# Optimization experiments

Hardware: AMD Instinct MI355X
Metric: run time of the kernel (lower is better)

The kernel has to match this reference:

```python
import jax, jax.numpy as jnp
import numpy as np

K = 1000   # grid rows (detections from model 1, truncated to 1000)
N = 1000   # grid cols (detections from model 2)
M = 900000 # number of non-empty (overlapping) pairs
F = 7      # per-pair feature dim
SENTINEL = -9999.0


def setup_inputs() -> dict:
    key = jax.random.key(0)
    ks = jax.random.split(key, 12)
    def w(k, o, i):
        return jax.random.normal(k, (o, i), dtype=jnp.float32) * 0.05
    def b(k, o):
        return jax.random.normal(k, (o,), dtype=jnp.float32) * 0.05
    return {
        "input_1": jax.random.normal(ks[0], (1, F, 1, M), dtype=jnp.float32),
        "T_out": jnp.zeros((1, K, N), dtype=jnp.float32),
        "T_indices": jax.random.randint(ks[1], (2, M), 0, K),
        "w1": w(ks[2], 18, F),  "b1": b(ks[3], 18),
        "w2": w(ks[4], 36, 18), "b2": b(ks[5], 36),
        "w3": w(ks[6], 36, 36), "b3": b(ks[7], 36),
        "w4": w(ks[8], 1, 36),  "b4": b(ks[9], 1),
    }


def reference(input_1, T_out, T_indices, w1, b1, w2, b2, w3, b3, w4, b4):
    # 1x1 conv stack == channel matmuls on the flattened [F, M] features.
    x = input_1[0, :, 0, :]                       # [F, M]
    h = jax.nn.relu(w1 @ x + b1[:, None])         # [18, M]
    h = jax.nn.relu(w2 @ h + b2[:, None])         # [36, M]
    h = jax.nn.relu(w3 @ h + b3[:, None])         # [36, M]
    vals = (w4 @ h + b4[:, None])[0]              # [M]

    grid = jnp.full(T_out.shape, SENTINEL, dtype=T_out.dtype)  # [1, K, N]
    grid = grid.at[:, T_indices[0], T_indices[1]].set(vals[None, :])

    # MaxPool2d([1, N]) -> max over cols; MaxPool2d([K, 1]) -> max over rows.
    row_max = grid.max(axis=2).squeeze()          # [K]
    col_max = grid.max(axis=1).squeeze()          # [N]
    return (row_max, col_max)
```

## Files before the change

### kernel.cpp

```cpp
#include <hip/hip_runtime.h>
#include <stdint.h>

#define KK 1000
#define NN 1000
#define MM 900000
#define FF 7
#define SENTINEL -9999.0f

template <int N, typename F>
__device__ __forceinline__ void unroll_loop(F&& f) {
    if constexpr (N > 0) {
        unroll_loop<N - 1>(static_cast<F&&>(f));
        f(N - 1);
    }
}

__global__ __launch_bounds__(256) void init_grid(ulonglong2* __restrict__ g, int n2) {
    int i = blockIdx.x * 256 + threadIdx.x;
    if (i < n2) g[i] = make_ulonglong2(0ULL, 0ULL);
}

__global__ __launch_bounds__(256, 4) void mlp_scatter(
    const float* __restrict__ in,
    const int*   __restrict__ idx,
    const float* __restrict__ w1, const float* __restrict__ b1,
    const float* __restrict__ w2, const float* __restrict__ b2,
    const float* __restrict__ w3, const float* __restrict__ b3,
    const float* __restrict__ w4, const float* __restrict__ b4,
    unsigned long long* __restrict__ grid)
{
    int m = blockIdx.x * 256 + threadIdx.x;
    if (m >= MM) return;

    float x[FF];
    unroll_loop<FF>([&](int f) { x[f] = in[f * MM + m]; });

    float h1[18];
    unroll_loop<18>([&](int o) {
        float a = b1[o];
        unroll_loop<FF>([&](int i) { a = fmaf(w1[o * FF + i], x[i], a); });
        h1[o] = fmaxf(a, 0.0f);
    });

    float h2[36];
    unroll_loop<36>([&](int o) {
        float a = b2[o];
        unroll_loop<18>([&](int i) { a = fmaf(w2[o * 18 + i], h1[i], a); });
        h2[o] = fmaxf(a, 0.0f);
    });

    float v = b4[0];
    unroll_loop<36>([&](int o) {
        float a = b3[o];
        unroll_loop<36>([&](int i) { a = fmaf(w3[o * 36 + i], h2[i], a); });
        v = fmaf(w4[o], fmaxf(a, 0.0f), v);
    });

    int r = idx[m];
    int c = idx[MM + m];
    unsigned long long packed =
        ((unsigned long long)(unsigned)(m + 1) << 32) | (unsigned)__float_as_uint(v);
    atomicMax(&grid[r * NN + c], packed);
}

__global__ __launch_bounds__(256) void row_max_k(const unsigned long long* __restrict__ g,
                                                 float* __restrict__ out) {
    int r = blockIdx.x;
    float mx = SENTINEL;
    for (int c = threadIdx.x; c < NN; c += 256) {
        unsigned long long p = g[(size_t)r * NN + c];
        if (p) mx = fmaxf(mx, __uint_as_float((unsigned)p));
    }
    __shared__ float red[256];
    red[threadIdx.x] = mx;
    __syncthreads();
    for (int s = 128; s > 0; s >>= 1) {
        if (threadIdx.x < s) red[threadIdx.x] = fmaxf(red[threadIdx.x], red[threadIdx.x + s]);
        __syncthreads();
    }
    if (threadIdx.x == 0) out[r] = red[0];
}

#define CCHUNKS 25
#define CROWS   (KK / CCHUNKS)

__global__ __launch_bounds__(256) void col_partial(const unsigned long long* __restrict__ g,
                                                   float* __restrict__ part) {
    int n = blockIdx.x * 256 + threadIdx.x;
    if (n >= NN) return;
    int k0 = blockIdx.y * CROWS;
    float mx = SENTINEL;
    for (int k = k0; k < k0 + CROWS; ++k) {
        unsigned long long p = g[(size_t)k * NN + n];
        if (p) mx = fmaxf(mx, __uint_as_float((unsigned)p));
    }
    part[blockIdx.y * NN + n] = mx;
}

__global__ __launch_bounds__(256) void col_final(const float* __restrict__ part,
                                                 float* __restrict__ out) {
    int n = blockIdx.x * 256 + threadIdx.x;
    if (n >= NN) return;
    float mx = SENTINEL;
#pragma unroll
    for (int c = 0; c < CCHUNKS; ++c) mx = fmaxf(mx, part[c * NN + n]);
    out[KK + n] = mx;
}

extern "C" void kernel_launch(void* const* d_in, const int* in_sizes, int n_in,
                              void* d_out, int out_size, void* d_ws, size_t ws_size,
                              hipStream_t stream) {
    const float* in  = (const float*)d_in[0];
    const int*   idx = (const int*)d_in[2];
    const float* w1  = (const float*)d_in[3];
    const float* b1  = (const float*)d_in[4];
    const float* w2  = (const float*)d_in[5];
    const float* b2  = (const float*)d_in[6];
    const float* w3  = (const float*)d_in[7];
    const float* b3  = (const float*)d_in[8];
    const float* w4  = (const float*)d_in[9];
    const float* b4  = (const float*)d_in[10];

    unsigned long long* grid = (unsigned long long*)d_ws;
    float* part = (float*)((char*)d_ws + (size_t)KK * NN * 8);
    float* out  = (float*)d_out;

    const int n2 = (KK * NN) / 2;
    init_grid<<<(n2 + 255) / 256, 256, 0, stream>>>((ulonglong2*)grid, n2);

    mlp_scatter<<<(MM + 255) / 256, 256, 0, stream>>>(
        in, idx, w1, b1, w2, b2, w3, b3, w4, b4, grid);

    row_max_k<<<KK, 256, 0, stream>>>(grid, out);
    col_partial<<<dim3(4, CCHUNKS), 256, 0, stream>>>(grid, part);
    col_final<<<4, 256, 0, stream>>>(part, out);
}
```

Measured before the change: 175.6 us.

## Process two pairs per thread in MLP and fuse row/col max kernels

Each MLP thread now evaluates two consecutive pairs. It uses float2/int2 loads and reuses each weight load for both pairs, and launch bounds drop to 3 waves per SIMD to allow the extra registers. The separate row-max, column-partial and column-final kernels become one kernel. Its column blocks combine partial results with a float atomicMax into an output that init_grid pre-fills with the sentinel. This saves two launches and the partial buffer, at the cost of higher register pressure and lower occupancy in the MLP kernel.

```diff
diff --git a/kernel.cpp b/kernel.cpp
--- a/kernel.cpp
+++ b/kernel.cpp
@@ -15,12 +15,14 @@
     }
 }
 
-__global__ __launch_bounds__(256) void init_grid(ulonglong2* __restrict__ g, int n2) {
+__global__ __launch_bounds__(256) void init_grid(ulonglong2* __restrict__ g, int n2,
+                                                 float* __restrict__ outcol) {
     int i = blockIdx.x * 256 + threadIdx.x;
     if (i < n2) g[i] = make_ulonglong2(0ULL, 0ULL);
+    if (i < NN) outcol[i] = SENTINEL;
 }
 
-__global__ __launch_bounds__(256, 4) void mlp_scatter(
+__global__ __launch_bounds__(256, 3) void mlp_scatter(
     const float* __restrict__ in,
     const int*   __restrict__ idx,
     const float* __restrict__ w1, const float* __restrict__ b1,
@@ -29,82 +31,93 @@
     const float* __restrict__ w4, const float* __restrict__ b4,
     unsigned long long* __restrict__ grid)
 {
-    int m = blockIdx.x * 256 + threadIdx.x;
-    if (m >= MM) return;
+    int t = blockIdx.x * 256 + threadIdx.x;
+    int m0 = t * 2;
+    if (m0 >= MM) return;
 
-    float x[FF];
-    unroll_loop<FF>([&](int f) { x[f] = in[f * MM + m]; });
-
-    float h1[18];
-    unroll_loop<18>([&](int o) {
-        float a = b1[o];
-        unroll_loop<FF>([&](int i) { a = fmaf(w1[o * FF + i], x[i], a); });
-        h1[o] = fmaxf(a, 0.0f);
+    float xa[FF], xb[FF];
+    unroll_loop<FF>([&](int f) {
+        float2 v = *reinterpret_cast<const float2*>(in + (size_t)f * MM + m0);
+        xa[f] = v.x; xb[f] = v.y;
     });
 
-    float h2[36];
-    unroll_loop<36>([&](int o) {
-        float a = b2[o];
-        unroll_loop<18>([&](int i) { a = fmaf(w2[o * 18 + i], h1[i], a); });
-        h2[o] = fmaxf(a, 0.0f);
+    float h1a[18], h1b[18];
+    unroll_loop<18>([&](int o) {
+        float a = b1[o], b = a;
+        unroll_loop<FF>([&](int i) {
+            float w_ = w1[o * FF + i];
+            a = fmaf(w_, xa[i], a); b = fmaf(w_, xb[i], b);
+        });
+        h1a[o] = fmaxf(a, 0.0f); h1b[o] = fmaxf(b, 0.0f);
     });
 
-    float v = b4[0];
+    float h2a[36], h2b[36];
     unroll_loop<36>([&](int o) {
-        float a = b3[o];
-        unroll_loop<36>([&](int i) { a = fmaf(w3[o * 36 + i], h2[i], a); });
-        v = fmaf(w4[o], fmaxf(a, 0.0f), v);
+        float a = b2[o], b = a;
+        unroll_loop<18>([&](int i) {
+            float w_ = w2[o * 18 + i];
+            a = fmaf(w_, h1a[i], a); b = fmaf(w_, h1b[i], b);
+        });
+        h2a[o] = fmaxf(a, 0.0f); h2b[o] = fmaxf(b, 0.0f);
     });
 
-    int r = idx[m];
-    int c = idx[MM + m];
-    unsigned long long packed =
-        ((unsigned long long)(unsigned)(m + 1) << 32) | (unsigned)__float_as_uint(v);
-    atomicMax(&grid[r * NN + c], packed);
-}
+    float va = b4[0], vb = va;
+    unroll_loop<36>([&](int o) {
+        float a = b3[o], b = a;
+        unroll_loop<36>([&](int i) {
+            float w_ = w3[o * 36 + i];
+            a = fmaf(w_, h2a[i], a); b = fmaf(w_, h2b[i], b);
+        });
+        float w4o = w4[o];
+        va = fmaf(w4o, fmaxf(a, 0.0f), va);
+        vb = fmaf(w4o, fmaxf(b, 0.0f), vb);
+    });
 
-__global__ __launch_bounds__(256) void row_max_k(const unsigned long long* __restrict__ g,
-                                                 float* __restrict__ out) {
-    int r = blockIdx.x;
-    float mx = SENTINEL;
-    for (int c = threadIdx.x; c < NN; c += 256) {
-        unsigned long long p = g[(size_t)r * NN + c];
-        if (p) mx = fmaxf(mx, __uint_as_float((unsigned)p));
-    }
-    __shared__ float red[256];
-    red[threadIdx.x] = mx;
-    __syncthreads();
-    for (int s = 128; s > 0; s >>= 1) {
-        if (threadIdx.x < s) red[threadIdx.x] = fmaxf(red[threadIdx.x], red[threadIdx.x + s]);
-        __syncthreads();
-    }
-    if (threadIdx.x == 0) out[r] = red[0];
+    int2 rr = *reinterpret_cast<const int2*>(idx + m0);
+    int2 cc = *reinterpret_cast<const int2*>(idx + MM + m0);
+    unsigned long long pa =
+        ((unsigned long long)(unsigned)(m0 + 1) << 32) | (unsigned)__float_as_uint(va);
+    unsigned long long pb =
+        ((unsigned long long)(unsigned)(m0 + 2) << 32) | (unsigned)__float_as_uint(vb);
+    atomicMax(&grid[rr.x * NN + cc.x], pa);
+    atomicMax(&grid[rr.y * NN + cc.y], pb);
 }
 
 #define CCHUNKS 25
 #define CROWS   (KK / CCHUNKS)
 
-__global__ __launch_bounds__(256) void col_partial(const unsigned long long* __restrict__ g,
-                                                   float* __restrict__ part) {
-    int n = blockIdx.x * 256 + threadIdx.x;
-    if (n >= NN) return;
-    int k0 = blockIdx.y * CROWS;
-    float mx = SENTINEL;
-    for (int k = k0; k < k0 + CROWS; ++k) {
-        unsigned long long p = g[(size_t)k * NN + n];
-        if (p) mx = fmaxf(mx, __uint_as_float((unsigned)p));
+__global__ __launch_bounds__(256) void maxes(const unsigned long long* __restrict__ g,
+                                             float* __restrict__ out) {
+    int b = blockIdx.x;
+    if (b < KK) {
+        int r = b;
+        float mx = SENTINEL;
+        for (int c = threadIdx.x; c < NN; c += 256) {
+            unsigned long long p = g[(size_t)r * NN + c];
+            if (p) mx = fmaxf(mx, __uint_as_float((unsigned)p));
+        }
+        __shared__ float red[256];
+        red[threadIdx.x] = mx;
+        __syncthreads();
+        for (int s = 128; s > 0; s >>= 1) {
+            if (threadIdx.x < s)
+                red[threadIdx.x] = fmaxf(red[threadIdx.x], red[threadIdx.x + s]);
+            __syncthreads();
+        }
+        if (threadIdx.x == 0) out[r] = red[0];
+    } else {
+        int cb = b - KK;
+        int n  = (cb & 3) * 256 + (int)threadIdx.x;
+        if (n < NN) {
+            int k0 = (cb >> 2) * CROWS;
+            float mx = SENTINEL;
+            for (int k = k0; k < k0 + CROWS; ++k) {
+                unsigned long long p = g[(size_t)k * NN + n];
+                if (p) mx = fmaxf(mx, __uint_as_float((unsigned)p));
+            }
+            atomicMax(out + KK + n, mx);
+        }
     }
-    part[blockIdx.y * NN + n] = mx;
-}
-
-__global__ __launch_bounds__(256) void col_final(const float* __restrict__ part,
-                                                 float* __restrict__ out) {
-    int n = blockIdx.x * 256 + threadIdx.x;
-    if (n >= NN) return;
-    float mx = SENTINEL;
-#pragma unroll
-    for (int c = 0; c < CCHUNKS; ++c) mx = fmaxf(mx, part[c * NN + n]);
-    out[KK + n] = mx;
 }
 
 extern "C" void kernel_launch(void* const* d_in, const int* in_sizes, int n_in,
@@ -122,16 +135,13 @@
     const float* b4  = (const float*)d_in[10];
 
     unsigned long long* grid = (unsigned long long*)d_ws;
-    float* part = (float*)((char*)d_ws + (size_t)KK * NN * 8);
-    float* out  = (float*)d_out;
+    float* out = (float*)d_out;
 
     const int n2 = (KK * NN) / 2;
-    init_grid<<<(n2 + 255) / 256, 256, 0, stream>>>((ulonglong2*)grid, n2);
+    init_grid<<<(n2 + 255) / 256, 256, 0, stream>>>((ulonglong2*)grid, n2, out + KK);
 
-    mlp_scatter<<<(MM + 255) / 256, 256, 0, stream>>>(
+    mlp_scatter<<<(MM / 2 + 255) / 256, 256, 0, stream>>>(
         in, idx, w1, b1, w2, b2, w3, b3, w4, b4, grid);
 
-    row_max_k<<<KK, 256, 0, stream>>>(grid, out);
-    col_partial<<<dim3(4, CCHUNKS), 256, 0, stream>>>(grid, part);
-    col_final<<<4, 256, 0, stream>>>(part, out);
+    maxes<<<KK + 100, 256, 0, stream>>>(grid, out);
 }
```

Measured after the change: 184.9 us. 1.05x slower.

## Use packed fp16 dot2 for MLP layers 2 and 3 with pre-packed weights

Applied to the files above, without the earlier changes.

Hidden activations are packed into fp16 pairs and layers 2 and 3 use the v_dot2 fp16 instruction with fp32 accumulation, which roughly halves the FMA instruction count in the compute-bound per-pair MLP. A small extra kernel converts w2 and w3 to packed half2 in workspace before the main kernel runs. This costs one extra launch and reduces activation and weight precision to fp16, which may shift the max values slightly against the fp32 reference.

```diff
diff --git a/kernel.cpp b/kernel.cpp
--- a/kernel.cpp
+++ b/kernel.cpp
@@ -7,11 +7,47 @@
 #define FF 7
 #define SENTINEL -9999.0f
 
+typedef _Float16 h2v __attribute__((ext_vector_type(2)));
+typedef __fp16  h2f __attribute__((ext_vector_type(2)));
+
 template <int N, typename F>
 __device__ __forceinline__ void unroll_loop(F&& f) {
     if constexpr (N > 0) {
         unroll_loop<N - 1>(static_cast<F&&>(f));
         f(N - 1);
+    }
+}
+
+#if __has_builtin(__builtin_amdgcn_fdot2)
+__device__ __forceinline__ float dot2(h2v a, h2v b, float c) {
+    return __builtin_amdgcn_fdot2(__builtin_bit_cast(h2f, a),
+                                  __builtin_bit_cast(h2f, b), c, false);
+}
+#else
+__device__ __forceinline__ float dot2(h2v a, h2v b, float c) {
+    return fmaf((float)a.x, (float)b.x, fmaf((float)a.y, (float)b.y, c));
+}
+#endif
+
+__device__ __forceinline__ h2v pkrtz(float a, float b) {
+#if __has_builtin(__builtin_amdgcn_cvt_pkrtz)
+    return __builtin_bit_cast(h2v, __builtin_amdgcn_cvt_pkrtz(a, b));
+#else
+    return h2v{(_Float16)a, (_Float16)b};
+#endif
+}
+
+__global__ __launch_bounds__(256) void pack_weights(
+    const float* __restrict__ w2, const float* __restrict__ w3,
+    h2v* __restrict__ w2h, h2v* __restrict__ w3h) {
+    int t = threadIdx.x;
+    for (int p = t; p < 36 * 9; p += 256) {
+        int o = p / 9, ip = p - o * 9;
+        w2h[p] = h2v{(_Float16)w2[o * 18 + 2 * ip], (_Float16)w2[o * 18 + 2 * ip + 1]};
+    }
+    for (int p = t; p < 36 * 18; p += 256) {
+        int o = p / 18, ip = p - o * 18;
+        w3h[p] = h2v{(_Float16)w3[o * 36 + 2 * ip], (_Float16)w3[o * 36 + 2 * ip + 1]};
     }
 }
 
@@ -24,8 +60,8 @@
     const float* __restrict__ in,
     const int*   __restrict__ idx,
     const float* __restrict__ w1, const float* __restrict__ b1,
-    const float* __restrict__ w2, const float* __restrict__ b2,
-    const float* __restrict__ w3, const float* __restrict__ b3,
+    const h2v*   __restrict__ w2h, const float* __restrict__ b2,
+    const h2v*   __restrict__ w3h, const float* __restrict__ b3,
     const float* __restrict__ w4, const float* __restrict__ b4,
     unsigned long long* __restrict__ grid)
 {
@@ -33,26 +69,32 @@
     if (m >= MM) return;
 
     float x[FF];
-    unroll_loop<FF>([&](int f) { x[f] = in[f * MM + m]; });
+    unroll_loop<FF>([&](int f) { x[f] = in[(size_t)f * MM + m]; });
 
-    float h1[18];
-    unroll_loop<18>([&](int o) {
-        float a = b1[o];
-        unroll_loop<FF>([&](int i) { a = fmaf(w1[o * FF + i], x[i], a); });
-        h1[o] = fmaxf(a, 0.0f);
+    h2v h1h[9];
+    unroll_loop<9>([&](int p) {
+        float a = b1[2 * p], b = b1[2 * p + 1];
+        unroll_loop<FF>([&](int i) {
+            a = fmaf(w1[(2 * p) * FF + i], x[i], a);
+            b = fmaf(w1[(2 * p + 1) * FF + i], x[i], b);
+        });
+        h1h[p] = pkrtz(fmaxf(a, 0.0f), fmaxf(b, 0.0f));
     });
 
-    float h2[36];
-    unroll_loop<36>([&](int o) {
-        float a = b2[o];
-        unroll_loop<18>([&](int i) { a = fmaf(w2[o * 18 + i], h1[i], a); });
-        h2[o] = fmaxf(a, 0.0f);
+    h2v h2h[18];
+    unroll_loop<18>([&](int p) {
+        float a = b2[2 * p], b = b2[2 * p + 1];
+        unroll_loop<9>([&](int ip) {
+            a = dot2(w2h[(2 * p) * 9 + ip], h1h[ip], a);
+            b = dot2(w2h[(2 * p + 1) * 9 + ip], h1h[ip], b);
+        });
+        h2h[p] = pkrtz(fmaxf(a, 0.0f), fmaxf(b, 0.0f));
     });
 
     float v = b4[0];
     unroll_loop<36>([&](int o) {
         float a = b3[o];
-        unroll_loop<36>([&](int i) { a = fmaf(w3[o * 36 + i], h2[i], a); });
+        unroll_loop<18>([&](int ip) { a = dot2(w3h[o * 18 + ip], h2h[ip], a); });
         v = fmaf(w4[o], fmaxf(a, 0.0f), v);
     });
 
@@ -123,13 +165,17 @@
 
     unsigned long long* grid = (unsigned long long*)d_ws;
     float* part = (float*)((char*)d_ws + (size_t)KK * NN * 8);
+    h2v* w2h = (h2v*)((char*)d_ws + (size_t)KK * NN * 8 + 100000);
+    h2v* w3h = (h2v*)((char*)d_ws + (size_t)KK * NN * 8 + 101296);
     float* out  = (float*)d_out;
+
+    pack_weights<<<1, 256, 0, stream>>>(w2, w3, w2h, w3h);
 
     const int n2 = (KK * NN) / 2;
     init_grid<<<(n2 + 255) / 256, 256, 0, stream>>>((ulonglong2*)grid, n2);
 
     mlp_scatter<<<(MM + 255) / 256, 256, 0, stream>>>(
-        in, idx, w1, b1, w2, b2, w3, b3, w4, b4, grid);
+        in, idx, w1, b1, w2h, b2, w3h, b3, w4, b4, grid);
 
     row_max_k<<<KK, 256, 0, stream>>>(grid, out);
     col_partial<<<dim3(4, CCHUNKS), 256, 0, stream>>>(grid, part);
```

After: 156.1 us. 11.1% less time.
